# Kernel tuning notes

Measured on AMD Instinct MI355X. Metric: run time of the kernel, lower is better.

## Reference

```python
import jax, jax.numpy as jnp
import numpy as np
from jax import lax

T, B, DIN, H, OUT, L = 256, 128, 20, 1024, 1095, 3


def setup_inputs() -> dict:
    key = jax.random.key(0)
    ks = jax.random.split(key, 8)
    x = jax.random.normal(ks[0], (T, B, DIN), dtype=jnp.float32)
    c = jnp.zeros((L, B, H), dtype=jnp.float32)  # accepted but unused, as in original
    s_in = 1.0 / np.sqrt(DIN)
    s_h = 1.0 / np.sqrt(H)
    W1 = jax.random.uniform(ks[1], (DIN, H), jnp.float32, -s_in, s_in)
    b1 = jnp.zeros((H,), jnp.float32)
    # SRU per-layer weights: W maps h -> [z | f_pre | r_pre] (3H); biases for f and r gates
    W_sru = jax.random.uniform(ks[2], (L, H, 3 * H), jnp.float32, -s_h, s_h)
    bf_sru = jnp.zeros((L, H), jnp.float32)
    br_sru = jnp.zeros((L, H), jnp.float32)
    W3 = jax.random.uniform(ks[3], (H, OUT), jnp.float32, -s_h, s_h)
    b3 = jnp.zeros((OUT,), jnp.float32)
    return {"x": x, "c": c, "W1": W1, "b1": b1, "W_sru": W_sru,
            "bf_sru": bf_sru, "br_sru": br_sru, "W3": W3, "b3": b3}


def _sru_layer(h, W, bf, br):
    """One SRU layer. h: (T,B,H). Returns (h_out (T,B,H), c_final (B,H))."""
    U = jnp.einsum('tbh,hk->tbk', h, W)                    # (T,B,3H) big GEMM up front
    z, f_pre, r_pre = jnp.split(U, 3, axis=-1)
    f = jax.nn.sigmoid(f_pre + bf)
    r = jax.nn.sigmoid(r_pre + br)

    def step(c_prev, inp):
        f_t, z_t, r_t, x_t = inp
        c_t = f_t * c_prev + (1.0 - f_t) * z_t
        h_t = r_t * c_t + (1.0 - r_t) * x_t               # highway (input_size == hidden_size)
        return c_t, h_t

    c0 = jnp.zeros(h.shape[1:], h.dtype)
    c_final, h_out = lax.scan(step, c0, (f, z, r, h))
    return h_out, c_final


def reference(x, c, W1, b1, W_sru, bf_sru, br_sru, W3, b3):
    t, b, _ = x.shape
    h = (x.reshape(t * b, -1) @ W1 + b1).reshape(t, b, H)  # Dense_layer1
    c_finals = []
    for l in range(L):                                      # 3 SRU layers (fixed count)
        h, c_l = _sru_layer(h, W_sru[l], bf_sru[l], br_sru[l])
        c_finals.append(c_l)
    out = h.reshape(t * b, H) @ W3 + b3                     # Dense_layer3 -> (T*B, OUT)
    return out, jnp.stack(c_finals)                         # ((T*B,OUT), (L,B,H))
```

## Files before the change

### kernel.cpp

```cpp
#include <hip/hip_runtime.h>
#include <hip/hip_bf16.h>


#define T_DIM 256
#define B_DIM 128
#define DIN 20
#define H_DIM 1024
#define OUT_DIM 1095
#define L_DIM 3
#define M_DIM (T_DIM * B_DIM)
#define H3 (3 * H_DIM)
#define OUT_ELEMS ((size_t)M_DIM * OUT_DIM)

typedef __bf16 bf16x8 __attribute__((ext_vector_type(8)));
typedef __bf16 bf16x4 __attribute__((ext_vector_type(4)));
typedef __bf16 bf16x2 __attribute__((ext_vector_type(2)));
typedef float f32x4 __attribute__((ext_vector_type(4)));

__device__ __forceinline__ void async16(const __bf16* g, __bf16* l) {
  __builtin_amdgcn_global_load_lds(
      (const __attribute__((address_space(1))) void*)g,
      (__attribute__((address_space(3))) void*)l, 16, 0, 0);
}

__global__ void transpose_sru(const float* __restrict__ W, __bf16* __restrict__ Wt) {
  __shared__ float tile[32][33];
  int l = blockIdx.z;
  int j0 = blockIdx.x * 32;
  int i0 = blockIdx.y * 32;
  int tx = threadIdx.x, ty = threadIdx.y;
  const float* Wl = W + (size_t)l * H_DIM * H3;
  __bf16* Wtl = Wt + (size_t)l * H_DIM * H3;
#pragma unroll
  for (int r = 0; r < 4; r++)
    tile[ty + r * 8][tx] = Wl[(size_t)(i0 + ty + r * 8) * H3 + j0 + tx];
  __syncthreads();
#pragma unroll
  for (int r = 0; r < 4; r++)
    Wtl[(size_t)(j0 + ty + r * 8) * H_DIM + i0 + tx] = (__bf16)tile[tx][ty + r * 8];
}

__global__ void transpose_w3(const float* __restrict__ W, __bf16* __restrict__ Wt) {
  __shared__ float tile[32][33];
  int j0 = blockIdx.x * 32;
  int i0 = blockIdx.y * 32;
  int tx = threadIdx.x, ty = threadIdx.y;
#pragma unroll
  for (int r = 0; r < 4; r++) {
    int j = j0 + tx;
    if (j < OUT_DIM)
      tile[ty + r * 8][tx] = W[(size_t)(i0 + ty + r * 8) * OUT_DIM + j];
  }
  __syncthreads();
#pragma unroll
  for (int r = 0; r < 4; r++) {
    int j = j0 + ty + r * 8;
    if (j < OUT_DIM)
      Wt[(size_t)j * H_DIM + i0 + tx] = (__bf16)tile[tx][ty + r * 8];
  }
}

__global__ __launch_bounds__(256) void dense1(const float* __restrict__ x,
                                              const float* __restrict__ W1,
                                              const float* __restrict__ b1,
                                              __bf16* __restrict__ h) {
  __shared__ float wsl[DIN * 256];
  __shared__ float xs[128 * DIN];
  int tid = threadIdx.x;
  int m0 = blockIdx.x * 128;
  int n0 = blockIdx.y * 256;
#pragma unroll
  for (int k = 0; k < DIN; k++) wsl[k * 256 + tid] = W1[k * H_DIM + n0 + tid];
  for (int idx = tid; idx < 128 * DIN; idx += 256) xs[idx] = x[(size_t)m0 * DIN + idx];
  __syncthreads();
  float wreg[DIN];
#pragma unroll
  for (int k = 0; k < DIN; k++) wreg[k] = wsl[k * 256 + tid];
  float bias = b1[n0 + tid];
  for (int m = 0; m < 128; m++) {
    float acc = bias;
#pragma unroll
    for (int k = 0; k < DIN; k++) acc += xs[m * DIN + k] * wreg[k];
    h[(size_t)(m0 + m) * H_DIM + n0 + tid] = (__bf16)acc;
  }
}


template <int MH, int EPI>
__device__ __forceinline__ void mfma16(f32x4 (&acc)[8][4], const bf16x8 (&aF)[4],
                                       const bf16x8 (&bF)[4]) {
  __builtin_amdgcn_s_setprio(1);
#pragma unroll
  for (int i = 0; i < 4; ++i)
#pragma unroll
    for (int fn = 0; fn < 4; ++fn) {
      if (EPI == 1)
        acc[MH * 4 + i][fn] =
            __builtin_amdgcn_mfma_f32_16x16x32_bf16(bF[fn], aF[i], acc[MH * 4 + i][fn], 0, 0, 0);
      else
        acc[MH * 4 + i][fn] =
            __builtin_amdgcn_mfma_f32_16x16x32_bf16(aF[i], bF[fn], acc[MH * 4 + i][fn], 0, 0, 0);
    }
  __builtin_amdgcn_s_setprio(0);
}

template <int EPI>
__global__ __launch_bounds__(512, 2) void gemm256(const __bf16* __restrict__ A,
                                                  const __bf16* __restrict__ Bt,
                                                  void* __restrict__ Cv,
                                                  const float* __restrict__ bias0,
                                                  const float* __restrict__ bias1,
                                                  int Ntotal, int ldc) {
  __shared__ __align__(16) char lds[131072];
  int tid = threadIdx.x;
  int lane = tid & 63;
  int w = tid >> 6;
  int wm = w & 1, wn = w >> 1;

  int gx = gridDim.x;
  int lin = blockIdx.y * gx + blockIdx.x;
  int xcd = lin & 7;
  int kk = lin >> 3;
  int bpx = gx >> 3;
  int sh = __builtin_ctz(bpx);
  int bx = xcd * bpx + (kk & (bpx - 1));
  int by = kk >> sh;
  int m0 = bx * 256, n0 = by * 256;

  int r8row = w * 8 + (lane >> 3);
  int cse = (((lane & 7) ^ (lane >> 3)) * 8);
  int l15 = lane & 15;
  int quad = lane >> 4;
  int asw = (lane & 7) << 4;

  f32x4 acc[8][4];
#pragma unroll
  for (int i = 0; i < 8; ++i)
#pragma unroll
    for (int j = 0; j < 4; ++j) acc[i][j] = (f32x4)0.f;
  bf16x8 aF[4], bF[4];

#define STAGE_TILE(T_) do { int _t = (T_); int _b = (_t & 1) * 65536;            \
    _Pragma("unroll") for (int _u = 0; _u < 4; ++_u)                             \
      async16(A + (size_t)(m0 + _u * 64 + r8row) * 1024 + _t * 64 + cse,         \
              (__bf16*)(lds + _b + _u * 8192 + w * 1024));                       \
    _Pragma("unroll") for (int _u = 0; _u < 4; ++_u) {                           \
      int _br = n0 + _u * 64 + r8row;                                            \
      if (EPI == 0 && _br > Ntotal - 1) _br = Ntotal - 1;                        \
      async16(Bt + (size_t)_br * 1024 + _t * 64 + cse,                           \
              (__bf16*)(lds + _b + 32768 + _u * 8192 + w * 1024));               \
    } } while (0)

#define LOAD_A(MH_, KS_) do {                                                    \
    _Pragma("unroll") for (int i = 0; i < 4; ++i)                                \
      aF[i] = *(const bf16x8*)(lds + bufc +                                      \
                (wm * 128 + (MH_) * 64 + i * 16 + l15) * 128 +                   \
                ((quad * 16 + (KS_) * 64) ^ asw)); } while (0)

#define LOAD_B(KS_) do {                                                         \
    _Pragma("unroll") for (int i = 0; i < 4; ++i)                                \
      bF[i] = *(const bf16x8*)(lds + bufc + 32768 +                              \
                (wn * 64 + i * 16 + l15) * 128 +                                 \
                ((quad * 16 + (KS_) * 64) ^ asw)); } while (0)

  STAGE_TILE(0);
  __syncthreads();

#pragma unroll 2
  for (int t = 0; t < 16; ++t) {
    int bufc = (t & 1) * 65536;
    if (t < 15) STAGE_TILE(t + 1);
    LOAD_B(0);
    LOAD_A(0, 0); mfma16<0, EPI>(acc, aF, bF);
    LOAD_A(1, 0); mfma16<1, EPI>(acc, aF, bF);
    LOAD_B(1);
    LOAD_A(0, 1); mfma16<0, EPI>(acc, aF, bF);
    LOAD_A(1, 1); mfma16<1, EPI>(acc, aF, bF);
    __syncthreads();
  }
#undef STAGE_TILE
#undef LOAD_A
#undef LOAD_B

  if (EPI == 1) {
    __bf16* U = (__bf16*)Cv;
    int gN[4];
    f32x4 bV[4];
#pragma unroll
    for (int fn = 0; fn < 4; ++fn) {
      int gc = n0 + wn * 64 + fn * 16 + quad * 4;
      int g = gc >> 10;
      gN[fn] = g;
      if (g == 1) bV[fn] = *(const f32x4*)&bias0[gc - 1024];
      else if (g == 2) bV[fn] = *(const f32x4*)&bias1[gc - 2048];
      else bV[fn] = (f32x4)0.f;
    }
#pragma unroll
    for (int fm = 0; fm < 8; ++fm) {
      int m = wm * 128 + fm * 16 + l15;
      char* rowp = lds + m * 512;
      int msw = (m & 7) << 4;
#pragma unroll
      for (int fn = 0; fn < 4; ++fn) {
        int nq = wn * 64 + fn * 16 + quad * 4;
        f32x4 v = acc[fm][fn];
        if (gN[fn] != 0) {
#pragma unroll
          for (int j = 0; j < 4; ++j) v[j] = 1.f / (1.f + __expf(-(v[j] + bV[fn][j])));
        }
        bf16x4 o;
#pragma unroll
        for (int j = 0; j < 4; ++j) o[j] = (__bf16)v[j];
        *(bf16x4*)(rowp + ((nq * 2) ^ msw)) = o;
      }
    }
    __syncthreads();
#pragma unroll
    for (int it = 0; it < 16; ++it) {
      int idx = it * 512 + tid;
      int row = idx >> 5;
      int ce = (idx & 31) * 8;
      bf16x8 val = *(const bf16x8*)(lds + row * 512 + ((ce * 2) ^ ((row & 7) << 4)));
      *(bf16x8*)&U[(size_t)(m0 + row) * ldc + n0 + ce] = val;
    }
  } else {
    float* C = (float*)Cv;
#pragma unroll
    for (int fm = 0; fm < 8; ++fm) {
      int rowBase = m0 + wm * 128 + fm * 16 + quad * 4;
#pragma unroll
      for (int fn = 0; fn < 4; ++fn) {
        int col = n0 + wn * 64 + fn * 16 + l15;
        if (col < Ntotal) {
          float badd = bias0[col];
#pragma unroll
          for (int r = 0; r < 4; ++r)
            C[(size_t)(rowBase + r) * ldc + col] = acc[fm][fn][r] + badd;
        }
      }
    }
  }
}

__global__ __launch_bounds__(256) void sru_scan(const __bf16* __restrict__ U,
                                                __bf16* __restrict__ h,
                                                float* __restrict__ cst,
                                                float* __restrict__ cfin,
                                                int tc, int first, int last) {
  int id = blockIdx.x * 256 + threadIdx.x;
  int n2 = id * 2;
  int b = n2 >> 10;
  int hh = n2 & 1023;
  float c0, c1;
  if (first) { c0 = 0.f; c1 = 0.f; }
  else { c0 = cst[n2]; c1 = cst[n2 + 1]; }
  size_t ub = (size_t)b * H3 + hh;
  size_t xb = (size_t)b * H_DIM + hh;
  const size_t strideU = (size_t)B_DIM * H3;
  const size_t strideH = (size_t)B_DIM * H_DIM;

  bf16x2 z2 = *(const bf16x2*)&U[ub];
  bf16x2 f2 = *(const bf16x2*)&U[ub + 1024];
  bf16x2 r2 = *(const bf16x2*)&U[ub + 2048];
  bf16x2 x2 = *(const bf16x2*)&h[xb];

  for (int t = 0; t < tc - 1; t++) {
    size_t ubn = ub + strideU, xbn = xb + strideH;
    bf16x2 z2n = *(const bf16x2*)&U[ubn];
    bf16x2 f2n = *(const bf16x2*)&U[ubn + 1024];
    bf16x2 r2n = *(const bf16x2*)&U[ubn + 2048];
    bf16x2 x2n = *(const bf16x2*)&h[xbn];

    float f0 = (float)f2[0], f1 = (float)f2[1];
    float r0 = (float)r2[0], r1 = (float)r2[1];
    c0 = f0 * c0 + (1.f - f0) * (float)z2[0];
    c1 = f1 * c1 + (1.f - f1) * (float)z2[1];
    float h0 = r0 * c0 + (1.f - r0) * (float)x2[0];
    float h1 = r1 * c1 + (1.f - r1) * (float)x2[1];
    bf16x2 o;
    o[0] = (__bf16)h0;
    o[1] = (__bf16)h1;
    *(bf16x2*)&h[xb] = o;

    z2 = z2n; f2 = f2n; r2 = r2n; x2 = x2n;
    ub = ubn; xb = xbn;
  }
  {
    float f0 = (float)f2[0], f1 = (float)f2[1];
    float r0 = (float)r2[0], r1 = (float)r2[1];
    c0 = f0 * c0 + (1.f - f0) * (float)z2[0];
    c1 = f1 * c1 + (1.f - f1) * (float)z2[1];
    float h0 = r0 * c0 + (1.f - r0) * (float)x2[0];
    float h1 = r1 * c1 + (1.f - r1) * (float)x2[1];
    bf16x2 o;
    o[0] = (__bf16)h0;
    o[1] = (__bf16)h1;
    *(bf16x2*)&h[xb] = o;
  }
  cst[n2] = c0;
  cst[n2 + 1] = c1;
  if (last) {
    cfin[n2] = c0;
    cfin[n2 + 1] = c1;
  }
}

extern "C" void kernel_launch(void* const* d_in, const int* in_sizes, int n_in,
                              void* d_out, int out_size, void* d_ws, size_t ws_size,
                              hipStream_t stream) {
  const float* x = (const float*)d_in[0];
  const float* W1 = (const float*)d_in[2];
  const float* b1 = (const float*)d_in[3];
  const float* Wsru = (const float*)d_in[4];
  const float* bf_s = (const float*)d_in[5];
  const float* br_s = (const float*)d_in[6];
  const float* W3 = (const float*)d_in[7];
  const float* b3 = (const float*)d_in[8];
  float* out = (float*)d_out;

  const size_t kFixed = 67108864ull + 18874368ull + 2242560ull + 524288ull;
  int tch = (ws_size >= kFixed + (size_t)128 * B_DIM * H3 * 2) ? 128 : 64;
  int mch = tch * B_DIM;
  int nch = T_DIM / tch;

  char* wsb = (char*)d_ws;
  __bf16* h = (__bf16*)(wsb);
  __bf16* U = (__bf16*)(wsb + 67108864);
  char* wAfter = wsb + 67108864 + (size_t)mch * H3 * 2;
  __bf16* Wt = (__bf16*)(wAfter);
  __bf16* W3t = (__bf16*)(wAfter + 18874368);
  float* cst = (float*)(wAfter + 18874368 + 2242560);

  transpose_sru<<<dim3(H3 / 32, H_DIM / 32, L_DIM), dim3(32, 8), 0, stream>>>(Wsru, Wt);
  transpose_w3<<<dim3((OUT_DIM + 31) / 32, H_DIM / 32), dim3(32, 8), 0, stream>>>(W3, W3t);
  dense1<<<dim3(M_DIM / 128, H_DIM / 256), 256, 0, stream>>>(x, W1, b1, h);

  for (int l = 0; l < L_DIM; l++) {
    const __bf16* Wtl = Wt + (size_t)l * H_DIM * H3;
    const float* bfl = bf_s + l * H_DIM;
    const float* brl = br_s + l * H_DIM;
    float* cfin = out + OUT_ELEMS + (size_t)l * B_DIM * H_DIM;
    for (int ch = 0; ch < nch; ch++) {
      __bf16* hA = h + (size_t)ch * mch * H_DIM;
      gemm256<1><<<dim3(mch / 256, H3 / 256), 512, 0, stream>>>(hA, Wtl, U, bfl, brl, H3, H3);
      sru_scan<<<dim3(B_DIM * H_DIM / 512), 256, 0, stream>>>(
          U, hA, cst, cfin, tch, ch == 0 ? 1 : 0, ch == (nch - 1) ? 1 : 0);
    }
  }

  gemm256<0><<<dim3(M_DIM / 256, (OUT_DIM + 255) / 256), 512, 0, stream>>>(
      h, W3t, out, b3, nullptr, OUT_DIM, OUT_DIM);
}
```

Baseline: 1.239 ms.

## Add 8-wave software-pipelined gate GEMM with XCD-aware block remap

Replaces the generic gemm256 for the SRU gate projection with a specialized kernel. It uses 8 waves, a phased ping-pong schedule that interleaves LDS reads, async global-to-LDS loads and MFMA groups between barriers, and XCD-aware block index remapping for L2 locality. The epilogue applies bias and sigmoid and stages the result through swizzled LDS for coalesced stores. The hand-tuned waitcnt and barrier schedule adds complexity and the risk of subtle race bugs. It also assumes K=1024 and a grid width divisible by 8.

```diff
diff --git a/kernel.cpp b/kernel.cpp
--- a/kernel.cpp
+++ b/kernel.cpp
@@ -23,6 +23,12 @@
       (__attribute__((address_space(3))) void*)l, 16, 0, 0);
 }
 
+__device__ __forceinline__ void bar() {
+  asm volatile("" ::: "memory");
+  __builtin_amdgcn_s_barrier();
+  asm volatile("" ::: "memory");
+}
+
 __global__ void transpose_sru(const float* __restrict__ W, __bf16* __restrict__ Wt) {
   __shared__ float tile[32][33];
   int l = blockIdx.z;
@@ -85,6 +91,171 @@
   }
 }
 
+
+__global__ __launch_bounds__(512, 2) void gemm_gate8(const __bf16* __restrict__ A,
+                                                     const __bf16* __restrict__ Bt,
+                                                     __bf16* __restrict__ U,
+                                                     const float* __restrict__ biasf,
+                                                     const float* __restrict__ biasr) {
+  __shared__ __align__(16) char lds[131072];
+  int tid = threadIdx.x;
+  int lane = tid & 63;
+  int w = tid >> 6;
+  int wm = w & 1, wn = w >> 1;
+
+  int gx = gridDim.x;
+  int lin = blockIdx.y * gx + blockIdx.x;
+  int xcd = lin & 7;
+  int kk = lin >> 3;
+  int bpx = gx >> 3;
+  int sh = __builtin_ctz(bpx);
+  int bx = xcd * bpx + (kk & (bpx - 1));
+  int by = kk >> sh;
+  int m0 = bx * 256, n0 = by * 256;
+
+  int sr = tid >> 3;
+  int sc = (((tid & 7) ^ ((tid >> 3) & 7)) * 8);
+  int l15 = lane & 15;
+  int quad = lane >> 4;
+  int asw = (lane & 7) << 4;
+
+  f32x4 acc[8][4];
+#pragma unroll
+  for (int i = 0; i < 8; ++i)
+#pragma unroll
+    for (int j = 0; j < 4; ++j) acc[i][j] = (f32x4)0.f;
+  bf16x8 Ar[4][2];
+  bf16x8 bA[8];
+  bf16x8 bB[8];
+
+#define LGK0 asm volatile("s_waitcnt lgkmcnt(0)" ::: "memory")
+#define VM4  asm volatile("s_waitcnt vmcnt(4)" ::: "memory")
+#define VM0  asm volatile("s_waitcnt vmcnt(0)" ::: "memory")
+
+#define RD_B(BS, BUFB) do {                                                      \
+    _Pragma("unroll") for (int fn = 0; fn < 4; ++fn)                             \
+    _Pragma("unroll") for (int ks = 0; ks < 2; ++ks)                             \
+      BS[fn * 2 + ks] = *(const bf16x8*)(lds + (BUFB) + 32768 +                  \
+          (wn * 64 + fn * 16 + l15) * 128 + ((quad * 16 + ks * 64) ^ asw));      \
+  } while (0)
+
+#define RD_A(BUFB, HI) do {                                                      \
+    _Pragma("unroll") for (int fm = 0; fm < 4; ++fm)                             \
+    _Pragma("unroll") for (int ks = 0; ks < 2; ++ks)                             \
+      Ar[fm][ks] = *(const bf16x8*)(lds + (BUFB) +                               \
+          (wm * 128 + (HI) * 64 + fm * 16 + l15) * 128 +                         \
+          ((quad * 16 + ks * 64) ^ asw));                                        \
+  } while (0)
+
+#define MM(KS, BS, FMO) do {                                                     \
+    __builtin_amdgcn_s_setprio(1);                                               \
+    _Pragma("unroll") for (int fm = 0; fm < 4; ++fm)                             \
+    _Pragma("unroll") for (int fn = 0; fn < 4; ++fn)                             \
+      acc[(FMO) + fm][fn] = __builtin_amdgcn_mfma_f32_16x16x32_bf16(             \
+          BS[fn * 2 + (KS)], Ar[fm][(KS)], acc[(FMO) + fm][fn], 0, 0, 0);        \
+    __builtin_amdgcn_s_setprio(0);                                               \
+  } while (0)
+
+#define ST_A(T_, H_) do { int _bb = ((T_) & 1) * 65536;                          \
+    const __bf16* _s = A + (size_t)(m0 + (H_) * 128 + sr) * 1024 + (T_) * 64 + sc; \
+    async16(_s, (__bf16*)(lds + _bb + (H_) * 16384 + tid * 16));                 \
+    async16(_s + (size_t)64 * 1024,                                              \
+            (__bf16*)(lds + _bb + (H_) * 16384 + 8192 + tid * 16)); } while (0)
+
+#define ST_B(T_, H_) do { int _bb = ((T_) & 1) * 65536;                          \
+    const __bf16* _s = Bt + (size_t)(n0 + (H_) * 128 + sr) * 1024 + (T_) * 64 + sc; \
+    async16(_s, (__bf16*)(lds + _bb + 32768 + (H_) * 16384 + tid * 16));         \
+    async16(_s + (size_t)64 * 1024,                                              \
+            (__bf16*)(lds + _bb + 32768 + (H_) * 16384 + 8192 + tid * 16)); } while (0)
+
+#define PH(RD_, ST_, MM_, VW_) do { RD_; ST_; VW_; bar(); LGK0; MM_; bar(); } while (0)
+#define NOP ((void)0)
+
+  ST_A(0, 0); ST_A(0, 1); ST_B(0, 0); ST_B(0, 1);
+  ST_B(1, 0); ST_B(1, 1);
+  VM4;
+  bar();
+
+  PH(RD_B(bA, 0),  ST_A(1, 0), NOP,          NOP);
+  PH(RD_A(0, 0),   ST_A(1, 1), MM(0, bA, 0), NOP);
+  PH(NOP,          ST_B(2, 0), MM(1, bA, 0), NOP);
+  PH(RD_A(0, 1),   ST_B(2, 1), MM(0, bA, 4), VM4);
+
+#define TILE_FULL(T_, BS, BSP) do {                                              \
+    PH(RD_B(BS, ((T_) & 1) * 65536), ST_A((T_) + 1, 0), MM(1, BSP, 4), NOP);     \
+    PH(RD_A(((T_) & 1) * 65536, 0),  ST_A((T_) + 1, 1), MM(0, BS, 0),  NOP);     \
+    PH(NOP,                          ST_B((T_) + 2, 0), MM(1, BS, 0),  NOP);     \
+    PH(RD_A(((T_) & 1) * 65536, 1),  ST_B((T_) + 2, 1), MM(0, BS, 4),  VM4);     \
+  } while (0)
+
+  for (int t2 = 1; t2 < 12; t2 += 2) {
+    TILE_FULL(t2, bB, bA);
+    TILE_FULL(t2 + 1, bA, bB);
+  }
+  TILE_FULL(13, bB, bA);
+  PH(RD_B(bA, 0),  ST_A(15, 0), MM(1, bB, 4), NOP);
+  PH(RD_A(0, 0),   ST_A(15, 1), MM(0, bA, 0), NOP);
+  PH(NOP,          NOP,         MM(1, bA, 0), NOP);
+  PH(RD_A(0, 1),   NOP,         MM(0, bA, 4), VM0);
+  PH(RD_B(bB, 65536), NOP, MM(1, bA, 4), NOP);
+  PH(RD_A(65536, 0),  NOP, MM(0, bB, 0), NOP);
+  PH(NOP,             NOP, MM(1, bB, 0), NOP);
+  PH(RD_A(65536, 1),  NOP, MM(0, bB, 4), NOP);
+  MM(1, bB, 4);
+
+#undef TILE_FULL
+#undef PH
+#undef NOP
+#undef RD_B
+#undef RD_A
+#undef MM
+#undef ST_A
+#undef ST_B
+#undef LGK0
+#undef VM4
+#undef VM0
+
+  bar();
+  int gN[4];
+  f32x4 bV[4];
+#pragma unroll
+  for (int fn = 0; fn < 4; ++fn) {
+    int gc = n0 + wn * 64 + fn * 16 + quad * 4;
+    int g = gc >> 10;
+    gN[fn] = g;
+    if (g == 1) bV[fn] = *(const f32x4*)&biasf[gc - 1024];
+    else if (g == 2) bV[fn] = *(const f32x4*)&biasr[gc - 2048];
+    else bV[fn] = (f32x4)0.f;
+  }
+#pragma unroll
+  for (int fm = 0; fm < 8; ++fm) {
+    int m = wm * 128 + fm * 16 + l15;
+    char* rowp = lds + m * 512;
+    int msw = (m & 7) << 4;
+#pragma unroll
+    for (int fn = 0; fn < 4; ++fn) {
+      int nq = wn * 64 + fn * 16 + quad * 4;
+      f32x4 v = acc[fm][fn];
+      if (gN[fn] != 0) {
+#pragma unroll
+        for (int j = 0; j < 4; ++j) v[j] = 1.f / (1.f + __expf(-(v[j] + bV[fn][j])));
+      }
+      bf16x4 o;
+#pragma unroll
+      for (int j = 0; j < 4; ++j) o[j] = (__bf16)v[j];
+      *(bf16x4*)(rowp + ((nq * 2) ^ msw)) = o;
+    }
+  }
+  __syncthreads();
+#pragma unroll
+  for (int it = 0; it < 16; ++it) {
+    int idx = it * 512 + tid;
+    int row = idx >> 5;
+    int ce = (idx & 31) * 8;
+    bf16x8 val = *(const bf16x8*)(lds + row * 512 + ((ce * 2) ^ ((row & 7) << 4)));
+    *(bf16x8*)&U[(size_t)(m0 + row) * H3 + n0 + ce] = val;
+  }
+}
 
 template <int MH, int EPI>
 __device__ __forceinline__ void mfma16(f32x4 (&acc)[8][4], const bf16x8 (&aF)[4],
@@ -342,7 +513,7 @@
     float* cfin = out + OUT_ELEMS + (size_t)l * B_DIM * H_DIM;
     for (int ch = 0; ch < nch; ch++) {
       __bf16* hA = h + (size_t)ch * mch * H_DIM;
-      gemm256<1><<<dim3(mch / 256, H3 / 256), 512, 0, stream>>>(hA, Wtl, U, bfl, brl, H3, H3);
+      gemm_gate8<<<dim3(mch / 256, H3 / 256), 512, 0, stream>>>(hA, Wtl, U, bfl, brl);
       sru_scan<<<dim3(B_DIM * H_DIM / 512), 256, 0, stream>>>(
           U, hA, cst, cfin, tch, ch == 0 ? 1 : 0, ch == (nch - 1) ? 1 : 0);
     }
```

Result: slower. 1.341 ms (+8.2%).
